# Kernel optimization log

Measured on AMD Instinct MI355X. Metric: run time of the kernel, lower is better.

## Reference

```python
import jax, jax.numpy as jnp
import numpy as np

EPS = 1e-5
GROUPS = 8

def setup_inputs() -> dict:
    key = jax.random.key(0)
    ks = jax.random.split(key, 7)
    b, c, h, w = 32, 256, 32, 32
    x = jax.random.normal(ks[0], (b, c, h, w), dtype=jnp.float32)
    gn_w = jax.random.normal(ks[1], (c,), dtype=jnp.float32) * 0.02 + 1.0
    gn_b = jax.random.normal(ks[2], (c,), dtype=jnp.float32) * 0.02
    qkv_w = jax.random.normal(ks[3], (3 * c, c), dtype=jnp.float32) / np.sqrt(c)
    qkv_b = jax.random.normal(ks[4], (3 * c,), dtype=jnp.float32) * 0.02
    out_w = jax.random.normal(ks[5], (c, c), dtype=jnp.float32) / np.sqrt(c)
    out_b = jax.random.normal(ks[6], (c,), dtype=jnp.float32) * 0.02
    return {"x": x, "gn_w": gn_w, "gn_b": gn_b, "qkv_w": qkv_w,
            "qkv_b": qkv_b, "out_w": out_w, "out_b": out_b}

def _group_norm(x, w, b):
    B, C, H, W = x.shape
    xg = x.reshape(B, GROUPS, C // GROUPS, H, W)
    mu = jnp.mean(xg, axis=(2, 3, 4), keepdims=True)
    var = jnp.var(xg, axis=(2, 3, 4), keepdims=True)
    xn = ((xg - mu) * jax.lax.rsqrt(var + EPS)).reshape(B, C, H, W)
    return xn * w[None, :, None, None] + b[None, :, None, None]

def reference(x, gn_w, gn_b, qkv_w, qkv_b, out_w, out_b):
    b, c, h, w = x.shape
    n = h * w
    xn = _group_norm(x, gn_w, gn_b)                       # [b,c,h,w]
    # 1x1 conv == channel matmul
    qkv = jnp.einsum('bchw,oc->bohw', xn, qkv_w) + qkv_b[None, :, None, None]
    q, k, v = jnp.split(qkv, 3, axis=1)                   # each [b,c,h,w]
    q = q.reshape(b, c, n).transpose(0, 2, 1)             # [b,n,c]
    k = k.reshape(b, c, n).transpose(0, 2, 1)
    v = v.reshape(b, c, n).transpose(0, 2, 1)
    scores = jnp.einsum('bnc,bmc->bnm', q, k) / jnp.sqrt(jnp.float32(c))
    attn = jax.nn.softmax(scores, axis=-1)                # [b,n,n]
    out = jnp.einsum('bnm,bmc->bnc', attn, v)             # [b,n,c]
    out = out.transpose(0, 2, 1).reshape(b, c, h, w)
    out = jnp.einsum('bchw,oc->bohw', out, out_w) + out_b[None, :, None, None]
    # NOTE: torch code reassigns x = group_norm(x), so residual is the normalized x
    return out + xn
```

## Files before the change

### kernel.cpp

```cpp
#include <hip/hip_runtime.h>
#include <hip/hip_bf16.h>

typedef __bf16 bf16;
typedef __bf16 bf16x4 __attribute__((ext_vector_type(4)));
typedef __bf16 bf16x8 __attribute__((ext_vector_type(8)));
typedef float f32x4 __attribute__((ext_vector_type(4)));

#define B_  32
#define C_  256
#define N_  1024
#define G_  8
#define CG_ 32
#define O3_ 768

#define SWZ9(el) ((el) ^ ((((el) >> 8) & 15) << 3))
#define SWZ7(el) ((el) ^ ((((el) >> 6) & 7) << 3))

#define GLOAD16(gp, lp)                                                        \
    __builtin_amdgcn_global_load_lds(                                          \
        (const __attribute__((address_space(1))) void*)(gp),                   \
        (__attribute__((address_space(3))) void*)(lp), 16, 0, 0)

__global__ __launch_bounds__(256) void k_convert(const float* __restrict__ qkv_w,
                                                 const float* __restrict__ out_w,
                                                 bf16* __restrict__ qkv_wh,
                                                 bf16* __restrict__ out_wh) {
    int i = blockIdx.x * 256 + threadIdx.x;
    if (i < O3_ * C_) qkv_wh[i] = (bf16)qkv_w[i];
    if (i < C_ * C_)  out_wh[i] = (bf16)out_w[i];
}

__global__ __launch_bounds__(256) void k_gn(const float* __restrict__ x,
                                            const float* __restrict__ w,
                                            const float* __restrict__ bia,
                                            bf16* __restrict__ xn,
                                            bf16* __restrict__ xt) {
    int bg = blockIdx.x;
    int b = bg >> 3, g = bg & 7;
    const float4* xb4 = (const float4*)(x + (size_t)b * C_ * N_ + (size_t)g * CG_ * N_);
    int tid = threadIdx.x;

    float s = 0.f, ss = 0.f;
    for (int i = tid; i < CG_ * N_ / 4; i += 256) {
        float4 v = xb4[i];
        s  += v.x + v.y + v.z + v.w;
        ss += v.x * v.x + v.y * v.y + v.z * v.z + v.w * v.w;
    }
    for (int off = 32; off; off >>= 1) {
        s  += __shfl_down(s, off);
        ss += __shfl_down(ss, off);
    }
    __shared__ float red[8];
    __shared__ float stat[2];
    int wid = tid >> 6, lane = tid & 63;
    if (lane == 0) { red[wid] = s; red[wid + 4] = ss; }
    __syncthreads();
    if (tid == 0) {
        float S  = red[0] + red[1] + red[2] + red[3];
        float SS = red[4] + red[5] + red[6] + red[7];
        float mu = S / (float)(CG_ * N_);
        float var = SS / (float)(CG_ * N_) - mu * mu;
        stat[0] = mu;
        stat[1] = rsqrtf(var + 1e-5f);
    }
    __syncthreads();
    float mu = stat[0], rstd = stat[1];

    __shared__ bf16 tile[256][CG_ + 8];
    for (int nc = 0; nc < N_; nc += 256) {
        for (int i = tid; i < 2048; i += 256) {
            int cl = i >> 6, f = i & 63;
            int c = g * CG_ + cl;
            float sc = rstd * w[c], sh = bia[c] - mu * sc;
            float4 v = xb4[(size_t)cl * 256 + (nc >> 2) + f];
            bf16x4 h = { (bf16)(v.x * sc + sh), (bf16)(v.y * sc + sh),
                         (bf16)(v.z * sc + sh), (bf16)(v.w * sc + sh) };
            *(bf16x4*)(xn + (size_t)b * C_ * N_ + (size_t)c * N_ + nc + f * 4) = h;
            tile[f * 4 + 0][cl] = h[0];
            tile[f * 4 + 1][cl] = h[1];
            tile[f * 4 + 2][cl] = h[2];
            tile[f * 4 + 3][cl] = h[3];
        }
        __syncthreads();
        for (int u = tid; u < 256 * 4; u += 256) {
            int nl = u >> 2, ch = u & 3;
            bf16x8 v = *(const bf16x8*)&tile[nl][ch * 8];
            *(bf16x8*)(xt + (size_t)b * N_ * C_ + (size_t)(nc + nl) * C_ + g * CG_ + ch * 8) = v;
        }
        __syncthreads();
    }
}

__global__ __launch_bounds__(256) void k_qkv(const bf16* __restrict__ xt,
                                             const bf16* __restrict__ wq,
                                             const float* __restrict__ qb,
                                             bf16* __restrict__ Qs,
                                             bf16* __restrict__ Kt,
                                             bf16* __restrict__ Vt) {
    __shared__ bf16 smem[17408];
    bf16* aT = smem;
    bf16* bT = smem + 8192;
    int nt = blockIdx.x, ot = blockIdx.y, b = blockIdx.z;
    int tid = threadIdx.x, wid = tid >> 6, lane = tid & 63;
    int wr = wid >> 1, wc = wid & 1;
    const bf16* Ab = xt + (size_t)b * N_ * C_ + (size_t)nt * 128 * C_;
    const bf16* Bb = wq + (size_t)ot * 128 * C_;

    bf16x8 areg[4], breg[4];
    #define LOAD_KT(kt)                                                        \
        for (int j = 0; j < 4; ++j) {                                          \
            int lin = (j * 256 + tid) * 8;                                     \
            int row = lin >> 6, col = lin & 63;                                \
            areg[j] = *(const bf16x8*)&Ab[(size_t)row * C_ + (kt) * 64 + col]; \
            breg[j] = *(const bf16x8*)&Bb[(size_t)row * C_ + (kt) * 64 + col]; \
        }

    f32x4 acc[4][4] = {};
    LOAD_KT(0);
    for (int kt = 0; kt < 4; ++kt) {
        for (int j = 0; j < 4; ++j) {
            int lin = (j * 256 + tid) * 8;
            *(bf16x8*)&aT[SWZ7(lin)] = areg[j];
            *(bf16x8*)&bT[SWZ7(lin)] = breg[j];
        }
        __syncthreads();
        if (kt < 3) { LOAD_KT(kt + 1); }
        for (int kk = 0; kk < 2; ++kk) {
            bf16x8 af[4], bfr[4];
            for (int m = 0; m < 4; ++m) {
                int el = (wr * 64 + m * 16 + (lane & 15)) * 64 + kk * 32 + (lane >> 4) * 8;
                af[m] = *(const bf16x8*)&aT[SWZ7(el)];
            }
            for (int n = 0; n < 4; ++n) {
                int el = (wc * 64 + n * 16 + (lane & 15)) * 64 + kk * 32 + (lane >> 4) * 8;
                bfr[n] = *(const bf16x8*)&bT[SWZ7(el)];
            }
            for (int m = 0; m < 4; ++m)
                for (int n = 0; n < 4; ++n)
                    acc[m][n] = __builtin_amdgcn_mfma_f32_16x16x32_bf16(af[m], bfr[n], acc[m][n], 0, 0, 0);
        }
        __syncthreads();
    }
    #undef LOAD_KT

    int o0 = ot * 128;
    if (ot < 4) {
        bf16* dst = (ot < 2) ? (Qs + (size_t)b * N_ * C_) : (Kt + (size_t)b * N_ * C_);
        float qsc = (ot < 2) ? 0.0625f : 1.0f;
        for (int m = 0; m < 4; ++m) for (int n = 0; n < 4; ++n) {
            int o = o0 + wc * 64 + n * 16 + (lane & 15);
            float bias = qb[o];
            int row0 = nt * 128 + wr * 64 + m * 16 + (lane >> 4) * 4;
            for (int r = 0; r < 4; ++r)
                dst[(size_t)(row0 + r) * C_ + (o & 255)] = (bf16)((acc[m][n][r] + bias) * qsc);
        }
    } else {
        bf16* tileE = smem;
        for (int m = 0; m < 4; ++m) for (int n = 0; n < 4; ++n) {
            int ol = wc * 64 + n * 16 + (lane & 15);
            float bias = qb[o0 + ol];
            int rl0 = wr * 64 + m * 16 + (lane >> 4) * 4;
            for (int r = 0; r < 4; ++r)
                tileE[(size_t)ol * 136 + rl0 + r] = (bf16)(acc[m][n][r] + bias);
        }
        __syncthreads();
        bf16* Vb = Vt + (size_t)b * C_ * N_ + (size_t)(o0 - 512) * N_ + (size_t)nt * 128;
        for (int u = tid; u < 128 * 16; u += 256) {
            int ol = u >> 4, ch = u & 15;
            bf16x8 v = *(const bf16x8*)&tileE[ol * 136 + ch * 8];
            *(bf16x8*)&Vb[(size_t)ol * N_ + ch * 8] = v;
        }
    }
}

__global__ __launch_bounds__(256, 2) void k_attn(const bf16* __restrict__ Qs,
                                                 const bf16* __restrict__ Kt,
                                                 const bf16* __restrict__ Vt,
                                                 bf16* __restrict__ Ao) {
    extern __shared__ char smem[];
    bf16*  kbuf = (bf16*)smem;
    bf16*  vbuf = (bf16*)(smem + 32768);
    bf16*  pl   = (bf16*)(smem + 65536);
    float* al   = (float*)(smem + 70656);
    int b = blockIdx.x, qb = blockIdx.y;
    int tid = threadIdx.x, wid = tid >> 6, lane = tid & 63;
    const bf16* Qb = Qs + (size_t)b * N_ * C_;
    const bf16* Kb = Kt + (size_t)b * N_ * C_;
    const bf16* Vb = Vt + (size_t)b * C_ * N_;
    int q0 = qb * 64;

    bf16x8 qf[8];
    {
        int row = q0 + wid * 16 + (lane & 15);
        const bf16* qr = Qb + (size_t)row * C_ + (lane >> 4) * 8;
        #pragma unroll
        for (int kk = 0; kk < 8; ++kk) qf[kk] = *(const bf16x8*)(qr + kk * 32);
    }

    f32x4 oac[4][4] = {};
    float lrun[4] = {0.f, 0.f, 0.f, 0.f};

    auto stage = [&](int mt, int bi) {
        int m0 = mt * 32;
        bf16* kd = kbuf + bi * 8192;
        bf16* vd = vbuf + bi * 8192;
        #pragma unroll
        for (int j = 0; j < 4; ++j) {
            int chunk = wid * 4 + j;
            int d = chunk * 512 + lane * 8;
            int ek = SWZ9(d);
            int krow = ek >> 8, kcol = ek & 255;
            GLOAD16(Kb + (size_t)(m0 + krow) * C_ + kcol, kd + chunk * 512);
            int ev = SWZ7(d);
            int kv = ev & 31;
            int ch = ((ev >> 6) << 1) | ((ev >> 5) & 1);
            GLOAD16(Vb + (size_t)ch * N_ + m0 + kv, vd + chunk * 512);
        }
    };

    stage(0, 0);
    __syncthreads();

    for (int mt = 0; mt < 32; ++mt) {
        int cur = mt & 1;
        if (mt < 31) stage(mt + 1, cur ^ 1);

        const bf16* kc = kbuf + cur * 8192;
        const bf16* vc = vbuf + cur * 8192;

        f32x4 sac[2] = {};
        __builtin_amdgcn_s_setprio(1);
        #pragma unroll
        for (int kk = 0; kk < 8; ++kk)
            #pragma unroll
            for (int n = 0; n < 2; ++n) {
                int el = (n * 16 + (lane & 15)) * 256 + kk * 32 + (lane >> 4) * 8;
                bf16x8 bfr = *(const bf16x8*)&kc[SWZ9(el)];
                sac[n] = __builtin_amdgcn_mfma_f32_16x16x32_bf16(qf[kk], bfr, sac[n], 0, 0, 0);
            }
        __builtin_amdgcn_s_setprio(0);

        #pragma unroll
        for (int r = 0; r < 4; ++r) {
            int prow = (wid * 16 + (lane >> 4) * 4 + r) * 40 + (lane & 15);
            float e0 = __expf(fminf(sac[0][r], 60.f));
            float e1 = __expf(fminf(sac[1][r], 60.f));
            lrun[r] += e0 + e1;
            pl[prow]      = (bf16)e0;
            pl[prow + 16] = (bf16)e1;
        }
        __syncthreads();

        __builtin_amdgcn_s_setprio(1);
        bf16x8 paf[4];
        #pragma unroll
        for (int m = 0; m < 4; ++m)
            paf[m] = *(const bf16x8*)&pl[(m * 16 + (lane & 15)) * 40 + (lane >> 4) * 8];
        #pragma unroll
        for (int n = 0; n < 4; ++n) {
            int ch = wid * 64 + n * 16 + (lane & 15);
            int e = (ch >> 1) * 64 + (ch & 1) * 32 + (lane >> 4) * 8;
            bf16x8 bfr = *(const bf16x8*)&vc[SWZ7(e)];
            #pragma unroll
            for (int m = 0; m < 4; ++m)
                oac[m][n] = __builtin_amdgcn_mfma_f32_16x16x32_bf16(paf[m], bfr, oac[m][n], 0, 0, 0);
        }
        __builtin_amdgcn_s_setprio(0);

        __syncthreads();
    }

    #pragma unroll
    for (int r = 0; r < 4; ++r) {
        float s = lrun[r];
        s += __shfl_xor(s, 1);
        s += __shfl_xor(s, 2);
        s += __shfl_xor(s, 4);
        s += __shfl_xor(s, 8);
        lrun[r] = s;
    }
    if (!(lane & 15)) {
        #pragma unroll
        for (int r = 0; r < 4; ++r)
            al[wid * 16 + (lane >> 4) * 4 + r] = 1.f / lrun[r];
    }
    __syncthreads();

    #pragma unroll
    for (int m = 0; m < 4; ++m)
        #pragma unroll
        for (int r = 0; r < 4; ++r) {
            float iv = al[m * 16 + (lane >> 4) * 4 + r];
            int row = q0 + m * 16 + (lane >> 4) * 4 + r;
            #pragma unroll
            for (int n = 0; n < 4; ++n)
                Ao[(size_t)b * N_ * C_ + (size_t)row * C_ + wid * 64 + n * 16 + (lane & 15)] =
                    (bf16)(oac[m][n][r] * iv);
        }
}

__global__ __launch_bounds__(256) void k_proj(const bf16* __restrict__ Ao,
                                              const bf16* __restrict__ wo,
                                              const float* __restrict__ ob,
                                              const bf16* __restrict__ xn,
                                              float* __restrict__ out) {
    __shared__ bf16 aT[128 * 64];
    __shared__ bf16 bT[128 * 64];
    int nt = blockIdx.x, ot = blockIdx.y, b = blockIdx.z;
    int tid = threadIdx.x, wid = tid >> 6, lane = tid & 63;
    int wr = wid >> 1, wc = wid & 1;
    const bf16* Abase = wo + (size_t)ot * 128 * C_;
    const bf16* Bbase = Ao + (size_t)b * N_ * C_ + (size_t)nt * 128 * C_;

    bf16x8 areg[4], breg[4];
    #define LOAD_KT(kt)                                                            \
        for (int j = 0; j < 4; ++j) {                                              \
            int lin = (j * 256 + tid) * 8;                                         \
            int row = lin >> 6, col = lin & 63;                                    \
            areg[j] = *(const bf16x8*)&Abase[(size_t)row * C_ + (kt) * 64 + col];  \
            breg[j] = *(const bf16x8*)&Bbase[(size_t)row * C_ + (kt) * 64 + col];  \
        }

    f32x4 acc[4][4] = {};
    LOAD_KT(0);
    for (int kt = 0; kt < 4; ++kt) {
        for (int j = 0; j < 4; ++j) {
            int lin = (j * 256 + tid) * 8;
            *(bf16x8*)&aT[SWZ7(lin)] = areg[j];
            *(bf16x8*)&bT[SWZ7(lin)] = breg[j];
        }
        __syncthreads();
        if (kt < 3) { LOAD_KT(kt + 1); }
        for (int kk = 0; kk < 2; ++kk) {
            bf16x8 af[4], bfr[4];
            for (int m = 0; m < 4; ++m) {
                int el = (wr * 64 + m * 16 + (lane & 15)) * 64 + kk * 32 + (lane >> 4) * 8;
                af[m] = *(const bf16x8*)&aT[SWZ7(el)];
            }
            for (int n = 0; n < 4; ++n) {
                int el = (wc * 64 + n * 16 + (lane & 15)) * 64 + kk * 32 + (lane >> 4) * 8;
                bfr[n] = *(const bf16x8*)&bT[SWZ7(el)];
            }
            for (int m = 0; m < 4; ++m)
                for (int n = 0; n < 4; ++n)
                    acc[m][n] = __builtin_amdgcn_mfma_f32_16x16x32_bf16(af[m], bfr[n], acc[m][n], 0, 0, 0);
        }
        __syncthreads();
    }
    #undef LOAD_KT

    for (int m = 0; m < 4; ++m) {
        int o0 = ot * 128 + wr * 64 + m * 16 + (lane >> 4) * 4;
        for (int n = 0; n < 4; ++n) {
            int col = nt * 128 + wc * 64 + n * 16 + (lane & 15);
            for (int r = 0; r < 4; ++r) {
                int o = o0 + r;
                float v = acc[m][n][r] + ob[o] + (float)xn[(size_t)b * C_ * N_ + (size_t)o * N_ + col];
                out[(size_t)b * C_ * N_ + (size_t)o * N_ + col] = v;
            }
        }
    }
}

extern "C" void kernel_launch(void* const* d_in, const int* in_sizes, int n_in,
                              void* d_out, int out_size, void* d_ws, size_t ws_size,
                              hipStream_t stream) {
    const float* x     = (const float*)d_in[0];
    const float* gn_w  = (const float*)d_in[1];
    const float* gn_b  = (const float*)d_in[2];
    const float* qkv_w = (const float*)d_in[3];
    const float* qkv_b = (const float*)d_in[4];
    const float* out_w = (const float*)d_in[5];
    const float* out_b = (const float*)d_in[6];
    float* out = (float*)d_out;

    char* ws = (char*)d_ws;
    size_t tensor = (size_t)B_ * C_ * N_ * 2;
    bf16* xn  = (bf16*)(ws);
    bf16* xt  = (bf16*)(ws + tensor);
    bf16* Qs  = (bf16*)(ws + 2 * tensor);
    bf16* Kt  = (bf16*)(ws + 3 * tensor);
    bf16* Vt  = (bf16*)(ws + 4 * tensor);
    bf16* Ao  = xt;
    bf16* qkv_wh = (bf16*)(ws + 5 * tensor);
    bf16* out_wh = (bf16*)(ws + 5 * tensor + (size_t)O3_ * C_ * 2);

    (void)hipFuncSetAttribute(reinterpret_cast<const void*>(&k_attn),
                              hipFuncAttributeMaxDynamicSharedMemorySize, 70912);

    k_convert<<<768, 256, 0, stream>>>(qkv_w, out_w, qkv_wh, out_wh);
    k_gn<<<256, 256, 0, stream>>>(x, gn_w, gn_b, xn, xt);
    k_qkv<<<dim3(8, 6, 32), 256, 0, stream>>>(xt, qkv_wh, qkv_b, Qs, Kt, Vt);
    k_attn<<<dim3(32, 16), 256, 70912, stream>>>(Qs, Kt, Vt, Ao);
    k_proj<<<dim3(8, 2, 32), 256, 0, stream>>>(Ao, out_wh, out_b, xn, out);
}
```

Measured before the change: 120.6 us.

## Use 64-key tiles and 32x32 MFMA for QK^T in attention kernel

The attention kernel now stages 64 keys per iteration instead of 32, which halves the loop trips and the barriers. QK^T switches to 32x32x16 MFMA, with warps split 2x2 across query and key halves. Row sums are combined across the two key-half warps through shared memory. LDS use roughly doubles to about 140KB and launch bounds drop to one block per CU, so occupancy falls while each iteration does more work.

```diff
diff --git a/kernel.cpp b/kernel.cpp
--- a/kernel.cpp
+++ b/kernel.cpp
@@ -5,6 +5,7 @@
 typedef __bf16 bf16x4 __attribute__((ext_vector_type(4)));
 typedef __bf16 bf16x8 __attribute__((ext_vector_type(8)));
 typedef float f32x4 __attribute__((ext_vector_type(4)));
+typedef float f32x16 __attribute__((ext_vector_type(16)));
 
 #define B_  32
 #define C_  256
@@ -14,6 +15,7 @@
 #define O3_ 768
 
 #define SWZ9(el) ((el) ^ ((((el) >> 8) & 15) << 3))
+#define SWZK(el) ((el) ^ ((((el) >> 8) & 31) << 3))
 #define SWZ7(el) ((el) ^ ((((el) >> 6) & 7) << 3))
 
 #define GLOAD16(gp, lp)                                                        \
@@ -173,47 +175,49 @@
     }
 }
 
-__global__ __launch_bounds__(256, 2) void k_attn(const bf16* __restrict__ Qs,
+__global__ __launch_bounds__(256, 1) void k_attn(const bf16* __restrict__ Qs,
                                                  const bf16* __restrict__ Kt,
                                                  const bf16* __restrict__ Vt,
                                                  bf16* __restrict__ Ao) {
     extern __shared__ char smem[];
     bf16*  kbuf = (bf16*)smem;
-    bf16*  vbuf = (bf16*)(smem + 32768);
-    bf16*  pl   = (bf16*)(smem + 65536);
-    float* al   = (float*)(smem + 70656);
+    bf16*  vbuf = (bf16*)(smem + 65536);
+    bf16*  pl   = (bf16*)(smem + 131072);
+    float* al   = (float*)(smem + 140288);
     int b = blockIdx.x, qb = blockIdx.y;
     int tid = threadIdx.x, wid = tid >> 6, lane = tid & 63;
+    int qh = wid >> 1, kvh = wid & 1;
+    int l31 = lane & 31, hi = lane >> 5;
     const bf16* Qb = Qs + (size_t)b * N_ * C_;
     const bf16* Kb = Kt + (size_t)b * N_ * C_;
     const bf16* Vb = Vt + (size_t)b * C_ * N_;
     int q0 = qb * 64;
 
-    bf16x8 qf[8];
+    bf16x8 qf[16];
     {
-        int row = q0 + wid * 16 + (lane & 15);
-        const bf16* qr = Qb + (size_t)row * C_ + (lane >> 4) * 8;
-        #pragma unroll
-        for (int kk = 0; kk < 8; ++kk) qf[kk] = *(const bf16x8*)(qr + kk * 32);
+        const bf16* qr = Qb + (size_t)(q0 + qh * 32 + l31) * C_ + hi * 8;
+        #pragma unroll
+        for (int kt = 0; kt < 16; ++kt) qf[kt] = *(const bf16x8*)(qr + kt * 16);
     }
 
     f32x4 oac[4][4] = {};
-    float lrun[4] = {0.f, 0.f, 0.f, 0.f};
+    float lrun[16];
+    #pragma unroll
+    for (int i = 0; i < 16; ++i) lrun[i] = 0.f;
 
     auto stage = [&](int mt, int bi) {
-        int m0 = mt * 32;
-        bf16* kd = kbuf + bi * 8192;
-        bf16* vd = vbuf + bi * 8192;
-        #pragma unroll
-        for (int j = 0; j < 4; ++j) {
-            int chunk = wid * 4 + j;
+        int m0 = mt * 64;
+        bf16* kd = kbuf + bi * 16384;
+        bf16* vd = vbuf + bi * 16384;
+        #pragma unroll
+        for (int j = 0; j < 8; ++j) {
+            int chunk = wid * 8 + j;
             int d = chunk * 512 + lane * 8;
-            int ek = SWZ9(d);
+            int ek = SWZK(d);
             int krow = ek >> 8, kcol = ek & 255;
             GLOAD16(Kb + (size_t)(m0 + krow) * C_ + kcol, kd + chunk * 512);
             int ev = SWZ7(d);
-            int kv = ev & 31;
-            int ch = ((ev >> 6) << 1) | ((ev >> 5) & 1);
+            int ch = ev >> 6, kv = ev & 63;
             GLOAD16(Vb + (size_t)ch * N_ + m0 + kv, vd + chunk * 512);
         }
     };
@@ -221,49 +225,51 @@
     stage(0, 0);
     __syncthreads();
 
-    for (int mt = 0; mt < 32; ++mt) {
+    for (int mt = 0; mt < 16; ++mt) {
         int cur = mt & 1;
-        if (mt < 31) stage(mt + 1, cur ^ 1);
-
-        const bf16* kc = kbuf + cur * 8192;
-        const bf16* vc = vbuf + cur * 8192;
-
-        f32x4 sac[2] = {};
+        if (mt < 15) stage(mt + 1, cur ^ 1);
+
+        const bf16* kc = kbuf + cur * 16384;
+        const bf16* vc = vbuf + cur * 16384;
+
+        f32x16 sac = {};
         __builtin_amdgcn_s_setprio(1);
         #pragma unroll
-        for (int kk = 0; kk < 8; ++kk)
+        for (int kt = 0; kt < 16; ++kt) {
+            int el = (kvh * 32 + l31) * 256 + kt * 16 + hi * 8;
+            bf16x8 kf = *(const bf16x8*)&kc[SWZK(el)];
+            sac = __builtin_amdgcn_mfma_f32_32x32x16_bf16(qf[kt], kf, sac, 0, 0, 0);
+        }
+        __builtin_amdgcn_s_setprio(0);
+
+        {
+            int pcol = kvh * 32 + l31;
             #pragma unroll
-            for (int n = 0; n < 2; ++n) {
-                int el = (n * 16 + (lane & 15)) * 256 + kk * 32 + (lane >> 4) * 8;
-                bf16x8 bfr = *(const bf16x8*)&kc[SWZ9(el)];
-                sac[n] = __builtin_amdgcn_mfma_f32_16x16x32_bf16(qf[kk], bfr, sac[n], 0, 0, 0);
-            }
-        __builtin_amdgcn_s_setprio(0);
-
-        #pragma unroll
-        for (int r = 0; r < 4; ++r) {
-            int prow = (wid * 16 + (lane >> 4) * 4 + r) * 40 + (lane & 15);
-            float e0 = __expf(fminf(sac[0][r], 60.f));
-            float e1 = __expf(fminf(sac[1][r], 60.f));
-            lrun[r] += e0 + e1;
-            pl[prow]      = (bf16)e0;
-            pl[prow + 16] = (bf16)e1;
+            for (int i = 0; i < 16; ++i) {
+                int prow = qh * 32 + (i & 3) + 8 * (i >> 2) + 4 * hi;
+                float e = __expf(fminf(sac[i], 60.f));
+                lrun[i] += e;
+                pl[prow * 72 + pcol] = (bf16)e;
+            }
         }
         __syncthreads();
 
         __builtin_amdgcn_s_setprio(1);
-        bf16x8 paf[4];
-        #pragma unroll
-        for (int m = 0; m < 4; ++m)
-            paf[m] = *(const bf16x8*)&pl[(m * 16 + (lane & 15)) * 40 + (lane >> 4) * 8];
-        #pragma unroll
-        for (int n = 0; n < 4; ++n) {
-            int ch = wid * 64 + n * 16 + (lane & 15);
-            int e = (ch >> 1) * 64 + (ch & 1) * 32 + (lane >> 4) * 8;
-            bf16x8 bfr = *(const bf16x8*)&vc[SWZ7(e)];
+        #pragma unroll
+        for (int ks = 0; ks < 2; ++ks) {
+            bf16x8 paf[4];
             #pragma unroll
             for (int m = 0; m < 4; ++m)
-                oac[m][n] = __builtin_amdgcn_mfma_f32_16x16x32_bf16(paf[m], bfr, oac[m][n], 0, 0, 0);
+                paf[m] = *(const bf16x8*)&pl[(m * 16 + (lane & 15)) * 72 + ks * 32 + (lane >> 4) * 8];
+            #pragma unroll
+            for (int n = 0; n < 4; ++n) {
+                int ch = wid * 64 + n * 16 + (lane & 15);
+                int e = ch * 64 + ks * 32 + (lane >> 4) * 8;
+                bf16x8 vf = *(const bf16x8*)&vc[SWZ7(e)];
+                #pragma unroll
+                for (int m = 0; m < 4; ++m)
+                    oac[m][n] = __builtin_amdgcn_mfma_f32_16x16x32_bf16(paf[m], vf, oac[m][n], 0, 0, 0);
+            }
         }
         __builtin_amdgcn_s_setprio(0);
 
@@ -271,18 +277,21 @@
     }
 
     #pragma unroll
-    for (int r = 0; r < 4; ++r) {
-        float s = lrun[r];
+    for (int i = 0; i < 16; ++i) {
+        float s = lrun[i];
         s += __shfl_xor(s, 1);
         s += __shfl_xor(s, 2);
         s += __shfl_xor(s, 4);
         s += __shfl_xor(s, 8);
-        lrun[r] = s;
-    }
-    if (!(lane & 15)) {
-        #pragma unroll
-        for (int r = 0; r < 4; ++r)
-            al[wid * 16 + (lane >> 4) * 4 + r] = 1.f / lrun[r];
+        s += __shfl_xor(s, 16);
+        lrun[i] = s;
+    }
+    if (l31 == 0) {
+        #pragma unroll
+        for (int i = 0; i < 16; ++i) {
+            int qrl = qh * 32 + (i & 3) + 8 * (i >> 2) + 4 * hi;
+            al[kvh * 64 + qrl] = lrun[i];
+        }
     }
     __syncthreads();
 
@@ -290,8 +299,9 @@
     for (int m = 0; m < 4; ++m)
         #pragma unroll
         for (int r = 0; r < 4; ++r) {
-            float iv = al[m * 16 + (lane >> 4) * 4 + r];
-            int row = q0 + m * 16 + (lane >> 4) * 4 + r;
+            int qrl = m * 16 + (lane >> 4) * 4 + r;
+            float iv = 1.f / (al[qrl] + al[64 + qrl]);
+            int row = q0 + qrl;
             #pragma unroll
             for (int n = 0; n < 4; ++n)
                 Ao[(size_t)b * N_ * C_ + (size_t)row * C_ + wid * 64 + n * 16 + (lane & 15)] =
@@ -386,11 +396,11 @@
     bf16* out_wh = (bf16*)(ws + 5 * tensor + (size_t)O3_ * C_ * 2);
 
     (void)hipFuncSetAttribute(reinterpret_cast<const void*>(&k_attn),
-                              hipFuncAttributeMaxDynamicSharedMemorySize, 70912);
+                              hipFuncAttributeMaxDynamicSharedMemorySize, 140800);
 
     k_convert<<<768, 256, 0, stream>>>(qkv_w, out_w, qkv_wh, out_wh);
     k_gn<<<256, 256, 0, stream>>>(x, gn_w, gn_b, xn, xt);
     k_qkv<<<dim3(8, 6, 32), 256, 0, stream>>>(xt, qkv_wh, qkv_b, Qs, Kt, Vt);
-    k_attn<<<dim3(32, 16), 256, 70912, stream>>>(Qs, Kt, Vt, Ao);
+    k_attn<<<dim3(32, 16), 256, 140800, stream>>>(Qs, Kt, Vt, Ao);
     k_proj<<<dim3(8, 2, 32), 256, 0, stream>>>(Ao, out_wh, out_b, xn, out);
 }
```

New measurement: 135.7 us. 1.13x slower.
